# Kernel optimization log

Measured on AMD Instinct MI355X. Metric: run time of the kernel, lower is better.

## Reference

```python
import jax, jax.numpy as jnp
import numpy as np

B, N, F, D, M, R, K, TOPR = 32, 1024, 10, 64, 4, 8, 20, 2
TAU = 1.0
BN_EPS = 1e-5


def setup_inputs() -> dict:
    key = jax.random.key(0)
    ks = jax.random.split(key, 20)
    s = 0.1
    p = {}
    p['data'] = jax.random.normal(ks[0], (B, N, F), jnp.float32)
    u = jnp.clip(jax.random.uniform(ks[1], (B, M), jnp.float32), 1e-6, 1.0 - 1e-6)
    p['gumbel_noise'] = -jnp.log(-jnp.log(u))
    p['W_cond'] = jax.random.normal(ks[2], (F, D), jnp.float32) * s
    p['b_cond'] = jnp.zeros((D,), jnp.float32)
    p['W_ap'] = jax.random.normal(ks[3], (D, D), jnp.float32) * s
    p['b_ap'] = jnp.zeros((D,), jnp.float32)
    p['W_av'] = jax.random.normal(ks[4], (D, 1), jnp.float32) * s
    p['W_r'] = jax.random.normal(ks[5], (D, M), jnp.float32) * s
    p['b_r'] = jnp.zeros((M,), jnp.float32)
    p['e_base'] = jax.random.normal(ks[6], (N, D), jnp.float32) * s
    p['lr_u'] = jax.random.normal(ks[7], (M, N, R), jnp.float32) * s
    p['lr_v'] = jax.random.normal(ks[8], (M, R, D), jnp.float32) * s
    p['W_gnn'] = jax.random.normal(ks[9], (F, D), jnp.float32) * s
    p['att_i'] = jax.random.normal(ks[10], (D,), jnp.float32) * s
    p['att_j'] = jax.random.normal(ks[11], (D,), jnp.float32) * s
    p['att_em_i'] = jax.random.normal(ks[12], (D,), jnp.float32) * s
    p['att_em_j'] = jax.random.normal(ks[13], (D,), jnp.float32) * s
    p['b_gnn'] = jnp.zeros((D,), jnp.float32)
    p['bn1_gamma'] = jnp.ones((D,), jnp.float32)
    p['bn1_beta'] = jnp.zeros((D,), jnp.float32)
    p['node_embed_table'] = jax.random.normal(ks[14], (N, D), jnp.float32) * s
    p['bn_out_gamma'] = jnp.ones((D,), jnp.float32)
    p['bn_out_beta'] = jnp.zeros((D,), jnp.float32)
    p['W_out'] = jax.random.normal(ks[15], (D, 1), jnp.float32) * s
    p['b_out'] = jnp.zeros((1,), jnp.float32)
    return p


def _nan(x):
    return jnp.nan_to_num(x, nan=0.0, posinf=1e4, neginf=-1e4)


def _bn(x, gamma, beta, axes):
    # BatchNorm1d in training mode: biased batch stats over `axes`.
    mu = x.mean(axes, keepdims=True)
    var = x.var(axes, keepdims=True)
    return (x - mu) * jax.lax.rsqrt(var + BN_EPS) * gamma + beta


def reference(data, gumbel_noise, W_cond, b_cond, W_ap, b_ap, W_av, W_r, b_r,
              e_base, lr_u, lr_v, W_gnn, att_i, att_j, att_em_i, att_em_j,
              b_gnn, bn1_gamma, bn1_beta, node_embed_table,
              bn_out_gamma, bn_out_beta, W_out, b_out):
    x_det = jax.lax.stop_gradient(data)                      # data.clone().detach()
    # --- condition attention pooling ---
    h_it = data @ W_cond + b_cond                            # [B,N,D]
    ah = jax.nn.leaky_relu(h_it @ W_ap + b_ap, 0.2)
    e_it = _nan((ah @ W_av)[..., 0])                         # [B,N]
    beta = jax.nn.softmax(e_it, axis=1)
    h_sys = jnp.sum(beta[..., None] * h_it, axis=1)          # [B,D]
    # --- gumbel top-k routing with straight-through ---
    pi_soft = jax.nn.softmax((h_sys @ W_r + b_r + gumbel_noise) / TAU, axis=-1)
    topv, topi = jax.lax.top_k(pi_soft, TOPR)
    pi_hard = jnp.sum(jax.nn.one_hot(topi, M, dtype=pi_soft.dtype) * topv[..., None], axis=1)
    pi_hard = pi_hard / jnp.maximum(pi_hard.sum(-1, keepdims=True), 1e-12)
    pi_t = jax.lax.stop_gradient(pi_hard - pi_soft) + pi_soft
    # --- low-rank expert prototypes -> mixed node embeddings ---
    proto = e_base[None] + jnp.einsum('mnr,mrd->mnd', lr_u, lr_v)    # [M,N,D]
    mixed = _nan(jnp.einsum('bm,mnd->bnd', pi_t, proto))             # [B,N,D]
    # --- dynamic top-k graph construction ---
    scores = _nan(jnp.einsum('bid,bjd->bij', mixed, mixed))          # [B,N,N]
    topk_vals, topk_idx = jax.lax.top_k(scores, K)                   # src nodes per dst: [B,N,K]
    topk_w = jax.nn.softmax(topk_vals, axis=-1)                      # edge weights
    # --- GAT-style layer with embedding-augmented keys, self loops re-added ---
    x_lin = x_det @ W_gnn                                            # [B,N,D]
    s_i = x_lin @ att_i + mixed @ att_em_i                           # [B,N]
    s_j = x_lin @ att_j + mixed @ att_em_j
    sj_nb = jnp.take_along_axis(s_j, topk_idx.reshape(B, N * K), axis=1).reshape(B, N, K)
    self_mask = topk_idx == jnp.arange(N)[None, :, None]             # remove_self_loops on topk edges
    alpha_nb = jnp.where(self_mask, -jnp.inf, jax.nn.leaky_relu(s_i[:, :, None] + sj_nb, 0.2))
    alpha_self = jax.nn.leaky_relu(s_i + s_j, 0.2)
    att = jax.nn.softmax(jnp.concatenate([alpha_nb, alpha_self[..., None]], axis=-1), axis=-1)
    w_nb = att[..., :K] * topk_w                                     # edge_weight modulation
    w_self = att[..., K]
    x_src = jnp.take_along_axis(x_lin, topk_idx.reshape(B, N * K)[..., None], axis=1).reshape(B, N, K, D)
    gnn = jnp.einsum('bnk,bnkd->bnd', w_nb, x_src) + w_self[..., None] * x_lin + b_gnn
    gnn = jax.nn.relu(_bn(gnn.reshape(B * N, D), bn1_gamma, bn1_beta, 0).reshape(B, N, D))
    # --- output head ---
    out = gnn * node_embed_table[None]                               # [B,N,D]
    out = jax.nn.relu(_bn(out, bn_out_gamma, bn_out_beta, (0, 1)))   # dropout = identity (eval)
    out = (out @ W_out + b_out).reshape(-1, N)                       # [B,N]
    return out, h_sys, pi_soft
```

## Files before the change

### kernel.cpp

```cpp
#include <hip/hip_runtime.h>
#include <math.h>

#define BB 32
#define NN 1024
#define FF 10
#define DD 64
#define MM 4
#define RR 8
#define KK 20
#define BNROWS (BB*NN)

#define OFF_HIT   0ull
#define OFF_XLIN  2097152ull
#define OFF_EIT   4194304ull
#define OFF_PIT   4227072ull
#define OFF_MIXED 4227200ull
#define OFF_SI    6324352ull
#define OFF_SJ    6357120ull
#define OFF_GNN   7700608ull
#define OFF_OUTP  9797760ull
#define OFF_STAT  11894912ull
#define OFF_SC    (OFF_STAT + 2560ull)

__device__ __forceinline__ float wave_sum(float v) {
    #pragma unroll
    for (int off = 32; off; off >>= 1) v += __shfl_xor(v, off);
    return v;
}
__device__ __forceinline__ float wave_max(float v) {
    #pragma unroll
    for (int off = 32; off; off >>= 1) v = fmaxf(v, __shfl_xor(v, off));
    return v;
}

__global__ __launch_bounds__(256) void k_rows(
    const float* __restrict__ data, const float* __restrict__ W_cond,
    const float* __restrict__ b_cond, const float* __restrict__ W_ap,
    const float* __restrict__ b_ap, const float* __restrict__ W_av,
    const float* __restrict__ W_gnn,
    float* __restrict__ h_it, float* __restrict__ x_lin, float* __restrict__ e_it,
    float* __restrict__ stats)
{
    if (blockIdx.x < 10) {
        int idx = blockIdx.x * 256 + threadIdx.x;
        if (idx < 2336) stats[idx] = 0.f;
    }
    int w = threadIdx.x >> 6, lane = threadIdx.x & 63;
    int r = blockIdx.x * 4 + w;
    const float* dr = data + r * FF;
    float df[FF];
    #pragma unroll
    for (int f = 0; f < FF; f++) df[f] = dr[f];
    float h = b_cond[lane], x = 0.f;
    #pragma unroll
    for (int f = 0; f < FF; f++) {
        h = fmaf(df[f], W_cond[f * DD + lane], h);
        x = fmaf(df[f], W_gnn[f * DD + lane], x);
    }
    h_it[r * DD + lane] = h;
    x_lin[r * DD + lane] = x;
    float acc = b_ap[lane];
    #pragma unroll
    for (int e2 = 0; e2 < DD; e2++)
        acc = fmaf(__shfl(h, e2), W_ap[e2 * DD + lane], acc);
    float lr = acc > 0.f ? acc : 0.2f * acc;
    float ep = wave_sum(lr * W_av[lane]);
    if (lane == 0) e_it[r] = ep;
}

__global__ __launch_bounds__(256) void k_pool2(
    const float* __restrict__ e_it, const float* __restrict__ h_it,
    float* __restrict__ num, float* __restrict__ den)
{
    int w = threadIdx.x >> 6, lane = threadIdx.x & 63;
    int b = blockIdx.x >> 3, ch = blockIdx.x & 7;
    int base = b * NN + ch * 128 + w * 32;
    float acc = 0.f, dn = 0.f;
    #pragma unroll 4
    for (int i = 0; i < 32; i++) {
        float e = e_it[base + i];
        float wgt = expf(e);
        acc = fmaf(wgt, h_it[(size_t)(base + i) * DD + lane], acc);
        dn += wgt;
    }
    __shared__ float pa[4][DD];
    __shared__ float pd[4];
    pa[w][lane] = acc;
    if (lane == 0) pd[w] = dn;
    __syncthreads();
    if (w == 0) {
        float s = pa[0][lane] + pa[1][lane] + pa[2][lane] + pa[3][lane];
        atomicAdd(&num[b * DD + lane], s);
        if (lane == 0) atomicAdd(&den[b], pd[0] + pd[1] + pd[2] + pd[3]);
    }
}

__global__ void k_route(const float* __restrict__ num, const float* __restrict__ den,
                        const float* __restrict__ W_r, const float* __restrict__ b_r,
                        const float* __restrict__ gumbel,
                        float* __restrict__ h_sys, float* __restrict__ pi_soft,
                        float* __restrict__ pi_t)
{
    int tid = threadIdx.x;
    for (int i = tid; i < BB * DD; i += 256)
        h_sys[i] = num[i] / den[i >> 6];
    if (tid >= BB) return;
    int b = tid;
    float inv = 1.0f / den[b];
    float lg[MM];
    #pragma unroll
    for (int m = 0; m < MM; m++) lg[m] = b_r[m] + gumbel[b * MM + m];
    for (int d = 0; d < DD; d++) {
        float hv = num[b * DD + d] * inv;
        #pragma unroll
        for (int m = 0; m < MM; m++) lg[m] = fmaf(hv, W_r[d * MM + m], lg[m]);
    }
    float mx = fmaxf(fmaxf(lg[0], lg[1]), fmaxf(lg[2], lg[3]));
    float s = 0.f, p[MM];
    #pragma unroll
    for (int m = 0; m < MM; m++) { p[m] = expf(lg[m] - mx); s += p[m]; }
    #pragma unroll
    for (int m = 0; m < MM; m++) { p[m] /= s; pi_soft[b * MM + m] = p[m]; }
    int i1 = 0; float v1 = p[0];
    #pragma unroll
    for (int m = 1; m < MM; m++) if (p[m] > v1) { v1 = p[m]; i1 = m; }
    int i2 = -1; float v2 = -1.f;
    #pragma unroll
    for (int m = 0; m < MM; m++) if (m != i1 && p[m] > v2) { v2 = p[m]; i2 = m; }
    float norm = fmaxf(v1 + v2, 1e-12f);
    #pragma unroll
    for (int m = 0; m < MM; m++)
        pi_t[b * MM + m] = (m == i1 ? v1 : (m == i2 ? v2 : 0.f)) / norm;
}

__global__ __launch_bounds__(256) void k_mixed(
    const float* __restrict__ e_base, const float* __restrict__ lr_u,
    const float* __restrict__ lr_v, const float* __restrict__ pi_t,
    const float* __restrict__ x_lin,
    const float* __restrict__ att_i, const float* __restrict__ att_j,
    const float* __restrict__ att_em_i, const float* __restrict__ att_em_j,
    float* __restrict__ mixed, float* __restrict__ s_i, float* __restrict__ s_j)
{
    int w = threadIdx.x >> 6, lane = threadIdx.x & 63;
    int r = blockIdx.x * 4 + w;
    int b = r >> 10, n = r & 1023;
    float LR[MM];
    #pragma unroll
    for (int m = 0; m < MM; m++) {
        float a = 0.f;
        #pragma unroll
        for (int rr = 0; rr < RR; rr++)
            a = fmaf(lr_u[(m * NN + n) * RR + rr], lr_v[(m * RR + rr) * DD + lane], a);
        LR[m] = a;
    }
    float eb = e_base[n * DD + lane];
    float mx = 0.f;
    #pragma unroll
    for (int m = 0; m < MM; m++) mx = fmaf(pi_t[b * MM + m], eb + LR[m], mx);
    mixed[(size_t)r * DD + lane] = mx;
    float x = x_lin[(size_t)r * DD + lane];
    float r1 = wave_sum(x * att_i[lane] + mx * att_em_i[lane]);
    float r2 = wave_sum(x * att_j[lane] + mx * att_em_j[lane]);
    if (lane == 0) { s_i[r] = r1; s_j[r] = r2; }
}

__global__ __launch_bounds__(256) void k_score(
    const float* __restrict__ mixed_chunk, float* __restrict__ sc)
{
    __shared__ float As[32 * 132];
    __shared__ float Bs[32 * 132];
    int t = threadIdx.x;
    int bb = blockIdx.x >> 6;
    int rr = blockIdx.x & 63;
    int it = rr >> 3, jt = rr & 7;
    int i0 = it * 128, j0 = jt * 128;
    const float* mb = mixed_chunk + (size_t)bb * NN * DD;

    int tx = t & 15, ty = t >> 4;
    float acc[8][8];
    #pragma unroll
    for (int a = 0; a < 8; a++)
        #pragma unroll
        for (int bj = 0; bj < 8; bj++) acc[a][bj] = 0.f;

    int rowi[4], qi[4], swi[4];
    #pragma unroll
    for (int c = 0; c < 4; c++) {
        int id = t + c * 256;
        rowi[c] = (id & 15) | ((id >> 7) << 4);
        qi[c] = (id >> 4) & 7;
        swi[c] = ((rowi[c] & 4) << 4) | ((rowi[c] >> 3) << 2) | (rowi[c] & 3);
    }

    float4 pa[4], pb[4];
    #pragma unroll
    for (int c = 0; c < 4; c++) {
        pa[c] = *(const float4*)(mb + (size_t)(i0 + rowi[c]) * DD + qi[c] * 4);
        pb[c] = *(const float4*)(mb + (size_t)(j0 + rowi[c]) * DD + qi[c] * 4);
    }
    for (int hh = 0; hh < 2; hh++) {
        if (hh) __syncthreads();
        #pragma unroll
        for (int c = 0; c < 4; c++) {
            int pos = qi[c] * 4 * 132 + swi[c];
            As[pos] = pa[c].x; As[pos + 132] = pa[c].y; As[pos + 264] = pa[c].z; As[pos + 396] = pa[c].w;
            Bs[pos] = pb[c].x; Bs[pos + 132] = pb[c].y; Bs[pos + 264] = pb[c].z; Bs[pos + 396] = pb[c].w;
        }
        __syncthreads();
        if (hh == 0) {
            #pragma unroll
            for (int c = 0; c < 4; c++) {
                pa[c] = *(const float4*)(mb + (size_t)(i0 + rowi[c]) * DD + 32 + qi[c] * 4);
                pb[c] = *(const float4*)(mb + (size_t)(j0 + rowi[c]) * DD + 32 + qi[c] * 4);
            }
        }
        #pragma unroll 4
        for (int d = 0; d < 32; d++) {
            float4 a0 = *(const float4*)&As[d * 132 + ty * 4];
            float4 a1 = *(const float4*)&As[d * 132 + 64 + ty * 4];
            float4 b0 = *(const float4*)&Bs[d * 132 + tx * 4];
            float4 b1 = *(const float4*)&Bs[d * 132 + 64 + tx * 4];
            float av[8] = {a0.x, a0.y, a0.z, a0.w, a1.x, a1.y, a1.z, a1.w};
            float bv[8] = {b0.x, b0.y, b0.z, b0.w, b1.x, b1.y, b1.z, b1.w};
            #pragma unroll
            for (int a = 0; a < 8; a++)
                #pragma unroll
                for (int bj = 0; bj < 8; bj++)
                    acc[a][bj] = fmaf(av[a], bv[bj], acc[a][bj]);
        }
    }

    float* out = sc + ((size_t)bb * NN + i0 + ty * 8) * NN + j0 + tx * 8;
    #pragma unroll
    for (int a = 0; a < 8; a++) {
        float4 o0 = {acc[a][0], acc[a][1], acc[a][2], acc[a][3]};
        float4 o1 = {acc[a][4], acc[a][5], acc[a][6], acc[a][7]};
        *(float4*)(out + (size_t)a * NN) = o0;
        *(float4*)(out + (size_t)a * NN + 4) = o1;
    }
}

__global__ __launch_bounds__(256) void k_selgat(
    const float* __restrict__ sc, int b0,
    const float* __restrict__ x_lin, const float* __restrict__ s_i,
    const float* __restrict__ s_j, const float* __restrict__ b_gnn,
    float* __restrict__ gnn_pre)
{
    int w = threadIdx.x >> 6, lane = threadIdx.x & 63;
    int lr = blockIdx.x * 4 + w;
    int r = b0 * NN + lr;
    int b = r >> 10, n = r & 1023;
    const float* row = sc + (size_t)lr * NN;

    unsigned uk[16];
    #pragma unroll
    for (int c = 0; c < 4; c++) {
        float4 v = *(const float4*)(row + c * 256 + lane * 4);
        float vv[4] = {v.x, v.y, v.z, v.w};
        #pragma unroll
        for (int q = 0; q < 4; q++) {
            unsigned u = __float_as_uint(vv[q]);
            uk[c * 4 + q] = u ^ (((unsigned)((int)u >> 31)) | 0x80000000u);
        }
    }
    unsigned mx = uk[0];
    #pragma unroll
    for (int i = 1; i < 16; i++) mx = uk[i] > mx ? uk[i] : mx;
    unsigned sv = mx;
    #pragma unroll
    for (int blk = 2; blk <= 64; blk <<= 1) {
        #pragma unroll
        for (int dist = blk >> 1; dist >= 1; dist >>= 1) {
            unsigned pv = (unsigned)__shfl_xor((int)sv, dist);
            bool up = (lane & blk) == 0;
            bool upper = (lane & dist) == 0;
            bool g = sv > pv;
            sv = (((g == upper) == up)) ? sv : pv;
        }
    }
    unsigned tau = (unsigned)__shfl((int)sv, 19);

    __shared__ unsigned skey[4][64];
    __shared__ int sjj[4][64];
    int base = 0;
    #pragma unroll
    for (int s = 0; s < 16; s++) {
        bool q = uk[s] >= tau;
        unsigned long long m = __ballot(q);
        if (q) {
            int pos = base + __popcll(m & ((1ull << lane) - 1ull));
            if (pos < 64) {
                skey[w][pos] = uk[s];
                sjj[w][pos] = ((s >> 2) << 8) + lane * 4 + (s & 3);
            }
        }
        base += __popcll(m);
    }
    int C = base;

    float vk = -INFINITY; int ik = 0;
    if (C <= 64) {
        unsigned ck = 0u; int cj = 0x7FFFFFFF;
        if (lane < C) { ck = skey[w][lane]; cj = sjj[w][lane]; }
        if (C <= 32) {
            #pragma unroll
            for (int blk = 2; blk <= 32; blk <<= 1)
                #pragma unroll
                for (int dist = blk >> 1; dist >= 1; dist >>= 1) {
                    unsigned pk = (unsigned)__shfl_xor((int)ck, dist);
                    int pj = __shfl_xor(cj, dist);
                    bool up = (lane & blk) == 0;
                    bool upper = (lane & dist) == 0;
                    bool g = (ck > pk) || (ck == pk && cj < pj);
                    bool keep = ((g == upper) == up);
                    ck = keep ? ck : pk; cj = keep ? cj : pj;
                }
        } else {
            #pragma unroll
            for (int blk = 2; blk <= 64; blk <<= 1)
                #pragma unroll
                for (int dist = blk >> 1; dist >= 1; dist >>= 1) {
                    unsigned pk = (unsigned)__shfl_xor((int)ck, dist);
                    int pj = __shfl_xor(cj, dist);
                    bool up = (lane & blk) == 0;
                    bool upper = (lane & dist) == 0;
                    bool g = (ck > pk) || (ck == pk && cj < pj);
                    bool keep = ((g == upper) == up);
                    ck = keep ? ck : pk; cj = keep ? cj : pj;
                }
        }
        if (lane < KK) {
            unsigned u = (ck & 0x80000000u) ? (ck ^ 0x80000000u) : ~ck;
            vk = __uint_as_float(u);
            ik = cj;
        }
    } else {
        for (int k = 0; k < KK; k++) {
            unsigned bm = uk[0]; int bsl = 0;
            #pragma unroll
            for (int i = 1; i < 16; i++) if (uk[i] > bm) { bm = uk[i]; bsl = i; }
            unsigned wm = bm;
            #pragma unroll
            for (int off = 32; off; off >>= 1) {
                unsigned tt = (unsigned)__shfl_xor((int)wm, off);
                wm = tt > wm ? tt : wm;
            }
            unsigned long long ball = __ballot(bm == wm);
            int winner = (int)__builtin_ctzll(ball);
            int slotw = __shfl(bsl, winner);
            int jw = ((slotw >> 2) << 8) + winner * 4 + (slotw & 3);
            unsigned u2 = (wm & 0x80000000u) ? (wm ^ 0x80000000u) : ~wm;
            if (lane == k) { vk = __uint_as_float(u2); ik = jw; }
            if (lane == winner) uk[bsl] = 0u;
        }
    }

    float m1 = wave_max(vk);
    float ek = (lane < KK) ? expf(vk - m1) : 0.f;
    float s1v = wave_sum(ek);
    float wk = ek / s1v;
    float si = s_i[r], sjn = s_j[r];
    float a = -INFINITY;
    if (lane < KK) {
        float sjk = s_j[(b << 10) + ik];
        float t2 = si + sjk;
        a = (ik == n) ? -INFINITY : (t2 > 0.f ? t2 : 0.2f * t2);
    }
    float ts = si + sjn;
    float aself = ts > 0.f ? ts : 0.2f * ts;
    float am = wave_max(fmaxf(a, aself));
    float ea = (lane < KK && a != -INFINITY) ? expf(a - am) : 0.f;
    float es = expf(aself - am);
    float ssum = wave_sum(ea) + es;
    float wnb = (ea / ssum) * wk;
    float wself = es / ssum;
    float acc = b_gnn[lane] + wself * x_lin[(size_t)r * DD + lane];
    #pragma unroll
    for (int k = 0; k < KK; k++) {
        int jk = __shfl(ik, k);
        float wv = __shfl(wnb, k);
        acc = fmaf(wv, x_lin[((size_t)(b << 10) + jk) * DD + lane], acc);
    }
    gnn_pre[(size_t)r * DD + lane] = acc;
}

__global__ __launch_bounds__(256) void k_stats(const float* __restrict__ src, float* __restrict__ sums)
{
    int w = threadIdx.x >> 6, lane = threadIdx.x & 63;
    __shared__ float ps[4][DD], pq[4][DD];
    float s = 0.f, q = 0.f;
    int base = blockIdx.x * 128;
    for (int i = w; i < 128; i += 4) {
        float v = src[(size_t)(base + i) * DD + lane];
        s += v; q = fmaf(v, v, q);
    }
    ps[w][lane] = s; pq[w][lane] = q;
    __syncthreads();
    if (w == 0) {
        s = ps[0][lane] + ps[1][lane] + ps[2][lane] + ps[3][lane];
        q = pq[0][lane] + pq[1][lane] + pq[2][lane] + pq[3][lane];
        atomicAdd(&sums[lane], s);
        atomicAdd(&sums[DD + lane], q);
    }
}

__global__ __launch_bounds__(256) void k_bn1(
    const float* __restrict__ gnn_pre, float* __restrict__ stats,
    const float* __restrict__ gamma, const float* __restrict__ beta,
    const float* __restrict__ net, float* __restrict__ out_pre)
{
    int tid = threadIdx.x;
    int d0 = (tid & 15) * 4;
    float mean4[4], rs4[4], bt4[4];
    #pragma unroll
    for (int k = 0; k < 4; k++) {
        float mu = stats[d0 + k] * (1.0f / BNROWS);
        float var = stats[64 + d0 + k] * (1.0f / BNROWS) - mu * mu;
        mean4[k] = mu;
        rs4[k] = rsqrtf(var + 1e-5f) * gamma[d0 + k];
        bt4[k] = beta[d0 + k];
    }
    float s4[4] = {0, 0, 0, 0}, q4[4] = {0, 0, 0, 0};
    size_t base4 = (size_t)blockIdx.x * 2048;
    #pragma unroll
    for (int i = 0; i < 8; i++) {
        size_t f4 = base4 + (size_t)i * 256 + tid;
        float4 v = ((const float4*)gnn_pre)[f4];
        int n = ((int)(f4 >> 4)) & 1023;
        float4 nv = ((const float4*)net)[(size_t)n * 16 + (tid & 15)];
        float vv[4] = {v.x, v.y, v.z, v.w};
        float nn2[4] = {nv.x, nv.y, nv.z, nv.w};
        float ov[4];
        #pragma unroll
        for (int k = 0; k < 4; k++) {
            float y = (vv[k] - mean4[k]) * rs4[k] + bt4[k];
            y = y > 0.f ? y : 0.f;
            float o = y * nn2[k];
            ov[k] = o;
            s4[k] += o;
            q4[k] = fmaf(o, o, q4[k]);
        }
        float4 o4 = {ov[0], ov[1], ov[2], ov[3]};
        ((float4*)out_pre)[f4] = o4;
    }
    __shared__ float4 ls[256], lq[256];
    ls[tid] = make_float4(s4[0], s4[1], s4[2], s4[3]);
    lq[tid] = make_float4(q4[0], q4[1], q4[2], q4[3]);
    __syncthreads();
    if (tid < 16) {
        float4 S = ls[tid], Q = lq[tid];
        #pragma unroll
        for (int rr = 1; rr < 16; rr++) {
            float4 a = ls[tid + 16 * rr], b = lq[tid + 16 * rr];
            S.x += a.x; S.y += a.y; S.z += a.z; S.w += a.w;
            Q.x += b.x; Q.y += b.y; Q.z += b.z; Q.w += b.w;
        }
        atomicAdd(&stats[128 + tid * 4 + 0], S.x);
        atomicAdd(&stats[128 + tid * 4 + 1], S.y);
        atomicAdd(&stats[128 + tid * 4 + 2], S.z);
        atomicAdd(&stats[128 + tid * 4 + 3], S.w);
        atomicAdd(&stats[192 + tid * 4 + 0], Q.x);
        atomicAdd(&stats[192 + tid * 4 + 1], Q.y);
        atomicAdd(&stats[192 + tid * 4 + 2], Q.z);
        atomicAdd(&stats[192 + tid * 4 + 3], Q.w);
    }
}

__global__ __launch_bounds__(256) void k_head(
    const float* __restrict__ out_pre, const float* __restrict__ stats,
    const float* __restrict__ gamma, const float* __restrict__ beta,
    const float* __restrict__ W_out, const float* __restrict__ b_out,
    float* __restrict__ out)
{
    int w = threadIdx.x >> 6, lane = threadIdx.x & 63;
    int r = blockIdx.x * 4 + w;
    float mean = stats[lane] * (1.0f / BNROWS);
    float var = stats[DD + lane] * (1.0f / BNROWS) - mean * mean;
    float rs = rsqrtf(var + 1e-5f);
    float y = (out_pre[(size_t)r * DD + lane] - mean) * rs * gamma[lane] + beta[lane];
    y = y > 0.f ? y : 0.f;
    float p = wave_sum(y * W_out[lane]);
    if (lane == 0) out[r] = p + b_out[0];
}

extern "C" void kernel_launch(void* const* d_in, const int* in_sizes, int n_in,
                              void* d_out, int out_size, void* d_ws, size_t ws_size,
                              hipStream_t stream)
{
    const float* data     = (const float*)d_in[0];
    const float* gumbel   = (const float*)d_in[1];
    const float* W_cond   = (const float*)d_in[2];
    const float* b_cond   = (const float*)d_in[3];
    const float* W_ap     = (const float*)d_in[4];
    const float* b_ap     = (const float*)d_in[5];
    const float* W_av     = (const float*)d_in[6];
    const float* W_r      = (const float*)d_in[7];
    const float* b_r      = (const float*)d_in[8];
    const float* e_base   = (const float*)d_in[9];
    const float* lr_u     = (const float*)d_in[10];
    const float* lr_v     = (const float*)d_in[11];
    const float* W_gnn    = (const float*)d_in[12];
    const float* att_i    = (const float*)d_in[13];
    const float* att_j    = (const float*)d_in[14];
    const float* att_em_i = (const float*)d_in[15];
    const float* att_em_j = (const float*)d_in[16];
    const float* b_gnn    = (const float*)d_in[17];
    const float* bn1_g    = (const float*)d_in[18];
    const float* bn1_b    = (const float*)d_in[19];
    const float* net      = (const float*)d_in[20];
    const float* bno_g    = (const float*)d_in[21];
    const float* bno_b    = (const float*)d_in[22];
    const float* W_out    = (const float*)d_in[23];
    const float* b_out    = (const float*)d_in[24];

    float* ws = (float*)d_ws;
    float* h_it   = ws + OFF_HIT;
    float* x_lin  = ws + OFF_XLIN;
    float* e_it   = ws + OFF_EIT;
    float* pi_t   = ws + OFF_PIT;
    float* mixed  = ws + OFF_MIXED;
    float* s_i    = ws + OFF_SI;
    float* s_j    = ws + OFF_SJ;
    float* gnn_pre = ws + OFF_GNN;
    float* out_pre = ws + OFF_OUTP;
    float* stats   = ws + OFF_STAT;
    float* pnum    = stats + 256;
    float* pden    = stats + 2304;

    float* out0    = (float*)d_out;
    float* h_sys   = out0 + BB * NN;
    float* pi_soft = out0 + BB * NN + BB * DD;

    k_rows<<<BNROWS / 4, 256, 0, stream>>>(data, W_cond, b_cond, W_ap, b_ap, W_av, W_gnn,
                                           h_it, x_lin, e_it, stats);
    k_pool2<<<BB * 8, 256, 0, stream>>>(e_it, h_it, pnum, pden);
    k_route<<<1, 256, 0, stream>>>(pnum, pden, W_r, b_r, gumbel, h_sys, pi_soft, pi_t);
    k_mixed<<<BNROWS / 4, 256, 0, stream>>>(e_base, lr_u, lr_v, pi_t, x_lin,
                                            att_i, att_j, att_em_i, att_em_j, mixed, s_i, s_j);

    size_t ws_floats = ws_size / 4;
    size_t avail = ws_floats > OFF_SC ? ws_floats - OFF_SC : 0;
    int cb = (int)(avail / (size_t)(NN * NN));
    if (cb > BB) cb = BB;
    float* sc = ws + OFF_SC;
    if (cb < 1) { cb = 2; sc = h_it; }
    for (int b0 = 0; b0 < BB; b0 += cb) {
        int c = (BB - b0) < cb ? (BB - b0) : cb;
        k_score<<<c * 64, 256, 0, stream>>>(mixed + (size_t)b0 * NN * DD, sc);
        k_selgat<<<c * 256, 256, 0, stream>>>(sc, b0, x_lin, s_i, s_j, b_gnn, gnn_pre);
    }

    k_stats<<<256, 256, 0, stream>>>(gnn_pre, stats);
    k_bn1<<<256, 256, 0, stream>>>(gnn_pre, stats, bn1_g, bn1_b, net, out_pre);
    k_head<<<BNROWS / 4, 256, 0, stream>>>(out_pre, stats + 128, bno_g, bno_b, W_out, b_out, out0);
}
```

Baseline: 327.1 us.

## Fuse score GEMM, top-k selection, GAT aggregation and BN stats into one kernel

Replaces the separate score GEMM, top-k/GAT kernel and stats kernel with one fused kernel. Each 512-thread block computes a 32x1024 similarity strip and keeps it in registers, with a transposed shared-memory B tile, then runs top-k, attention and aggregation directly on those registers. Batch-norm sums are accumulated in the same kernel. This removes the large N×N score matrix round trip through global memory and two kernel launches. In exchange it uses a large shared-memory footprint and 64 accumulators per thread, which may limit occupancy, and the transposed shared-memory stores may hit bank conflicts.

Measured after the change: 373.6 us. 14.2% more time.

```diff
diff --git a/kernel.cpp b/kernel.cpp
--- a/kernel.cpp
+++ b/kernel.cpp
@@ -20,7 +20,6 @@
 #define OFF_GNN   7700608ull
 #define OFF_OUTP  9797760ull
 #define OFF_STAT  11894912ull
-#define OFF_SC    (OFF_STAT + 2560ull)
 
 __device__ __forceinline__ float wave_sum(float v) {
     #pragma unroll
@@ -164,243 +163,223 @@
     if (lane == 0) { s_i[r] = r1; s_j[r] = r2; }
 }
 
-__global__ __launch_bounds__(256) void k_score(
-    const float* __restrict__ mixed_chunk, float* __restrict__ sc)
-{
-    __shared__ float As[32 * 132];
-    __shared__ float Bs[32 * 132];
+__global__ __launch_bounds__(512) void k_fused(
+    const float* __restrict__ mixed, const float* __restrict__ x_lin,
+    const float* __restrict__ s_i, const float* __restrict__ s_j,
+    const float* __restrict__ b_gnn, float* __restrict__ gnn_pre,
+    float* __restrict__ stats)
+{
+    __shared__ float As[32 * DD];
+    __shared__ float BT[DD * 256];
+
     int t = threadIdx.x;
-    int bb = blockIdx.x >> 6;
-    int rr = blockIdx.x & 63;
-    int it = rr >> 3, jt = rr & 7;
-    int i0 = it * 128, j0 = jt * 128;
-    const float* mb = mixed_chunk + (size_t)bb * NN * DD;
-
-    int tx = t & 15, ty = t >> 4;
-    float acc[8][8];
-    #pragma unroll
-    for (int a = 0; a < 8; a++)
-        #pragma unroll
-        for (int bj = 0; bj < 8; bj++) acc[a][bj] = 0.f;
-
-    int rowi[4], qi[4], swi[4];
+    int w = t >> 6, lane = t & 63;
+    int b = blockIdx.x >> 5;
+    int it = blockIdx.x & 31;
+    int i0 = it * 32;
+    const float* mb = mixed + (size_t)b * NN * DD;
+
+    *(float4*)&As[t * 4] = *(const float4*)(mb + (size_t)i0 * DD + t * 4);
+
+    float acc[4][16];
+    #pragma unroll
+    for (int a = 0; a < 4; a++)
+        #pragma unroll
+        for (int s = 0; s < 16; s++) acc[a][s] = 0.f;
+
+    int jl = t >> 1;
+    int dh = (t & 1) * 32;
+    int rbase = w * 4;
+
+    const float4* BT4 = (const float4*)BT;
+    const float4* As4 = (const float4*)As;
+
     #pragma unroll
     for (int c = 0; c < 4; c++) {
-        int id = t + c * 256;
-        rowi[c] = (id & 15) | ((id >> 7) << 4);
-        qi[c] = (id >> 4) & 7;
-        swi[c] = ((rowi[c] & 4) << 4) | ((rowi[c] >> 3) << 2) | (rowi[c] & 3);
-    }
-
-    float4 pa[4], pb[4];
-    #pragma unroll
-    for (int c = 0; c < 4; c++) {
-        pa[c] = *(const float4*)(mb + (size_t)(i0 + rowi[c]) * DD + qi[c] * 4);
-        pb[c] = *(const float4*)(mb + (size_t)(j0 + rowi[c]) * DD + qi[c] * 4);
-    }
-    for (int hh = 0; hh < 2; hh++) {
-        if (hh) __syncthreads();
-        #pragma unroll
-        for (int c = 0; c < 4; c++) {
-            int pos = qi[c] * 4 * 132 + swi[c];
-            As[pos] = pa[c].x; As[pos + 132] = pa[c].y; As[pos + 264] = pa[c].z; As[pos + 396] = pa[c].w;
-            Bs[pos] = pb[c].x; Bs[pos + 132] = pb[c].y; Bs[pos + 264] = pb[c].z; Bs[pos + 396] = pb[c].w;
-        }
         __syncthreads();
-        if (hh == 0) {
+        const float* src = mb + (size_t)(c * 256 + jl) * DD + dh;
+        #pragma unroll
+        for (int i = 0; i < 8; i++) {
+            float4 v = *(const float4*)(src + i * 4);
+            int d0 = dh + i * 4;
+            BT[(d0 + 0) * 256 + jl] = v.x;
+            BT[(d0 + 1) * 256 + jl] = v.y;
+            BT[(d0 + 2) * 256 + jl] = v.z;
+            BT[(d0 + 3) * 256 + jl] = v.w;
+        }
+        __syncthreads();
+        #pragma unroll 4
+        for (int d4 = 0; d4 < 16; d4++) {
+            float4 b0 = BT4[(d4 * 4 + 0) * 64 + lane];
+            float4 b1 = BT4[(d4 * 4 + 1) * 64 + lane];
+            float4 b2 = BT4[(d4 * 4 + 2) * 64 + lane];
+            float4 b3 = BT4[(d4 * 4 + 3) * 64 + lane];
             #pragma unroll
-            for (int c = 0; c < 4; c++) {
-                pa[c] = *(const float4*)(mb + (size_t)(i0 + rowi[c]) * DD + 32 + qi[c] * 4);
-                pb[c] = *(const float4*)(mb + (size_t)(j0 + rowi[c]) * DD + 32 + qi[c] * 4);
-            }
-        }
-        #pragma unroll 4
-        for (int d = 0; d < 32; d++) {
-            float4 a0 = *(const float4*)&As[d * 132 + ty * 4];
-            float4 a1 = *(const float4*)&As[d * 132 + 64 + ty * 4];
-            float4 b0 = *(const float4*)&Bs[d * 132 + tx * 4];
-            float4 b1 = *(const float4*)&Bs[d * 132 + 64 + tx * 4];
-            float av[8] = {a0.x, a0.y, a0.z, a0.w, a1.x, a1.y, a1.z, a1.w};
-            float bv[8] = {b0.x, b0.y, b0.z, b0.w, b1.x, b1.y, b1.z, b1.w};
+            for (int rr = 0; rr < 4; rr++) {
+                float4 a = As4[(rbase + rr) * 16 + d4];
+                acc[rr][c * 4 + 0] = fmaf(a.w, b3.x, fmaf(a.z, b2.x, fmaf(a.y, b1.x, fmaf(a.x, b0.x, acc[rr][c * 4 + 0]))));
+                acc[rr][c * 4 + 1] = fmaf(a.w, b3.y, fmaf(a.z, b2.y, fmaf(a.y, b1.y, fmaf(a.x, b0.y, acc[rr][c * 4 + 1]))));
+                acc[rr][c * 4 + 2] = fmaf(a.w, b3.z, fmaf(a.z, b2.z, fmaf(a.y, b1.z, fmaf(a.x, b0.z, acc[rr][c * 4 + 2]))));
+                acc[rr][c * 4 + 3] = fmaf(a.w, b3.w, fmaf(a.z, b2.w, fmaf(a.y, b1.w, fmaf(a.x, b0.w, acc[rr][c * 4 + 3]))));
+            }
+        }
+    }
+    __syncthreads();
+
+    unsigned* skeyW = (unsigned*)&BT[w * 64];
+    int*      sjjW  = (int*)&BT[512 + w * 64];
+
+    float ssum = 0.f, qsum = 0.f;
+
+    #pragma unroll 1
+    for (int rr = 0; rr < 4; rr++) {
+        int n = i0 + rbase + rr;
+        int r = (b << 10) + n;
+
+        unsigned uk[16];
+        #define EXTRACT_ROW(RRC) \
+            _Pragma("unroll") \
+            for (int s = 0; s < 16; s++) { \
+                unsigned u = __float_as_uint(acc[RRC][s]); \
+                uk[s] = u ^ (((unsigned)((int)u >> 31)) | 0x80000000u); \
+            }
+        if (rr == 0)      { EXTRACT_ROW(0) }
+        else if (rr == 1) { EXTRACT_ROW(1) }
+        else if (rr == 2) { EXTRACT_ROW(2) }
+        else              { EXTRACT_ROW(3) }
+
+        unsigned mx = uk[0];
+        #pragma unroll
+        for (int i = 1; i < 16; i++) mx = uk[i] > mx ? uk[i] : mx;
+        unsigned sv = mx;
+        #pragma unroll
+        for (int blk = 2; blk <= 64; blk <<= 1) {
             #pragma unroll
-            for (int a = 0; a < 8; a++)
+            for (int dist = blk >> 1; dist >= 1; dist >>= 1) {
+                unsigned pv = (unsigned)__shfl_xor((int)sv, dist);
+                bool up = (lane & blk) == 0;
+                bool upper = (lane & dist) == 0;
+                bool gt = sv > pv;
+                sv = ((gt == upper) == up) ? sv : pv;
+            }
+        }
+        unsigned tau = (unsigned)__shfl((int)sv, 19);
+
+        int base = 0;
+        #pragma unroll
+        for (int s = 0; s < 16; s++) {
+            bool q = uk[s] >= tau;
+            unsigned long long m = __ballot(q);
+            if (q) {
+                int pos = base + __popcll(m & ((1ull << lane) - 1ull));
+                if (pos < 64) {
+                    skeyW[pos] = uk[s];
+                    sjjW[pos] = ((s >> 2) << 8) + lane * 4 + (s & 3);
+                }
+            }
+            base += __popcll(m);
+        }
+        int C = base;
+
+        float vk = -INFINITY; int ik = 0;
+        if (C <= 64) {
+            unsigned ck = 0u; int cj = 0x7FFFFFFF;
+            if (lane < C) { ck = skeyW[lane]; cj = sjjW[lane]; }
+            if (C <= 32) {
                 #pragma unroll
-                for (int bj = 0; bj < 8; bj++)
-                    acc[a][bj] = fmaf(av[a], bv[bj], acc[a][bj]);
-        }
-    }
-
-    float* out = sc + ((size_t)bb * NN + i0 + ty * 8) * NN + j0 + tx * 8;
-    #pragma unroll
-    for (int a = 0; a < 8; a++) {
-        float4 o0 = {acc[a][0], acc[a][1], acc[a][2], acc[a][3]};
-        float4 o1 = {acc[a][4], acc[a][5], acc[a][6], acc[a][7]};
-        *(float4*)(out + (size_t)a * NN) = o0;
-        *(float4*)(out + (size_t)a * NN + 4) = o1;
-    }
-}
-
-__global__ __launch_bounds__(256) void k_selgat(
-    const float* __restrict__ sc, int b0,
-    const float* __restrict__ x_lin, const float* __restrict__ s_i,
-    const float* __restrict__ s_j, const float* __restrict__ b_gnn,
-    float* __restrict__ gnn_pre)
-{
-    int w = threadIdx.x >> 6, lane = threadIdx.x & 63;
-    int lr = blockIdx.x * 4 + w;
-    int r = b0 * NN + lr;
-    int b = r >> 10, n = r & 1023;
-    const float* row = sc + (size_t)lr * NN;
-
-    unsigned uk[16];
-    #pragma unroll
-    for (int c = 0; c < 4; c++) {
-        float4 v = *(const float4*)(row + c * 256 + lane * 4);
-        float vv[4] = {v.x, v.y, v.z, v.w};
-        #pragma unroll
-        for (int q = 0; q < 4; q++) {
-            unsigned u = __float_as_uint(vv[q]);
-            uk[c * 4 + q] = u ^ (((unsigned)((int)u >> 31)) | 0x80000000u);
-        }
-    }
-    unsigned mx = uk[0];
-    #pragma unroll
-    for (int i = 1; i < 16; i++) mx = uk[i] > mx ? uk[i] : mx;
-    unsigned sv = mx;
-    #pragma unroll
-    for (int blk = 2; blk <= 64; blk <<= 1) {
-        #pragma unroll
-        for (int dist = blk >> 1; dist >= 1; dist >>= 1) {
-            unsigned pv = (unsigned)__shfl_xor((int)sv, dist);
-            bool up = (lane & blk) == 0;
-            bool upper = (lane & dist) == 0;
-            bool g = sv > pv;
-            sv = (((g == upper) == up)) ? sv : pv;
-        }
-    }
-    unsigned tau = (unsigned)__shfl((int)sv, 19);
-
-    __shared__ unsigned skey[4][64];
-    __shared__ int sjj[4][64];
-    int base = 0;
-    #pragma unroll
-    for (int s = 0; s < 16; s++) {
-        bool q = uk[s] >= tau;
-        unsigned long long m = __ballot(q);
-        if (q) {
-            int pos = base + __popcll(m & ((1ull << lane) - 1ull));
-            if (pos < 64) {
-                skey[w][pos] = uk[s];
-                sjj[w][pos] = ((s >> 2) << 8) + lane * 4 + (s & 3);
-            }
-        }
-        base += __popcll(m);
-    }
-    int C = base;
-
-    float vk = -INFINITY; int ik = 0;
-    if (C <= 64) {
-        unsigned ck = 0u; int cj = 0x7FFFFFFF;
-        if (lane < C) { ck = skey[w][lane]; cj = sjj[w][lane]; }
-        if (C <= 32) {
-            #pragma unroll
-            for (int blk = 2; blk <= 32; blk <<= 1)
+                for (int blk = 2; blk <= 32; blk <<= 1)
+                    #pragma unroll
+                    for (int dist = blk >> 1; dist >= 1; dist >>= 1) {
+                        unsigned pk = (unsigned)__shfl_xor((int)ck, dist);
+                        int pj = __shfl_xor(cj, dist);
+                        bool up = (lane & blk) == 0;
+                        bool upper = (lane & dist) == 0;
+                        bool gt = (ck > pk) || (ck == pk && cj < pj);
+                        bool keep = ((gt == upper) == up);
+                        ck = keep ? ck : pk; cj = keep ? cj : pj;
+                    }
+            } else {
                 #pragma unroll
-                for (int dist = blk >> 1; dist >= 1; dist >>= 1) {
-                    unsigned pk = (unsigned)__shfl_xor((int)ck, dist);
-                    int pj = __shfl_xor(cj, dist);
-                    bool up = (lane & blk) == 0;
-                    bool upper = (lane & dist) == 0;
-                    bool g = (ck > pk) || (ck == pk && cj < pj);
-                    bool keep = ((g == upper) == up);
-                    ck = keep ? ck : pk; cj = keep ? cj : pj;
+                for (int blk = 2; blk <= 64; blk <<= 1)
+                    #pragma unroll
+                    for (int dist = blk >> 1; dist >= 1; dist >>= 1) {
+                        unsigned pk = (unsigned)__shfl_xor((int)ck, dist);
+                        int pj = __shfl_xor(cj, dist);
+                        bool up = (lane & blk) == 0;
+                        bool upper = (lane & dist) == 0;
+                        bool gt = (ck > pk) || (ck == pk && cj < pj);
+                        bool keep = ((gt == upper) == up);
+                        ck = keep ? ck : pk; cj = keep ? cj : pj;
+                    }
+            }
+            if (lane < KK) {
+                unsigned u = (ck & 0x80000000u) ? (ck ^ 0x80000000u) : ~ck;
+                vk = __uint_as_float(u);
+                ik = cj;
+            }
+        } else {
+            for (int k = 0; k < KK; k++) {
+                unsigned bm = uk[0]; int bsl = 0;
+                #pragma unroll
+                for (int i = 1; i < 16; i++) if (uk[i] > bm) { bm = uk[i]; bsl = i; }
+                unsigned wm = bm;
+                #pragma unroll
+                for (int off = 32; off; off >>= 1) {
+                    unsigned tt = (unsigned)__shfl_xor((int)wm, off);
+                    wm = tt > wm ? tt : wm;
                 }
-        } else {
-            #pragma unroll
-            for (int blk = 2; blk <= 64; blk <<= 1)
-                #pragma unroll
-                for (int dist = blk >> 1; dist >= 1; dist >>= 1) {
-                    unsigned pk = (unsigned)__shfl_xor((int)ck, dist);
-                    int pj = __shfl_xor(cj, dist);
-                    bool up = (lane & blk) == 0;
-                    bool upper = (lane & dist) == 0;
-                    bool g = (ck > pk) || (ck == pk && cj < pj);
-                    bool keep = ((g == upper) == up);
-                    ck = keep ? ck : pk; cj = keep ? cj : pj;
-                }
-        }
+                unsigned long long ball = __ballot(bm == wm);
+                int winner = (int)__builtin_ctzll(ball);
+                int slotw = __shfl(bsl, winner);
+                int jw = ((slotw >> 2) << 8) + winner * 4 + (slotw & 3);
+                unsigned u2 = (wm & 0x80000000u) ? (wm ^ 0x80000000u) : ~wm;
+                if (lane == k) { vk = __uint_as_float(u2); ik = jw; }
+                if (lane == winner) uk[bsl] = 0u;
+            }
+        }
+
+        float m1 = wave_max(vk);
+        float ek = (lane < KK) ? expf(vk - m1) : 0.f;
+        float s1v = wave_sum(ek);
+        float wk = ek / s1v;
+        float si = s_i[r], sjn = s_j[r];
+        float a = -INFINITY;
         if (lane < KK) {
-            unsigned u = (ck & 0x80000000u) ? (ck ^ 0x80000000u) : ~ck;
-            vk = __uint_as_float(u);
-            ik = cj;
-        }
-    } else {
+            float sjk = s_j[(b << 10) + ik];
+            float t2 = si + sjk;
+            a = (ik == n) ? -INFINITY : (t2 > 0.f ? t2 : 0.2f * t2);
+        }
+        float ts = si + sjn;
+        float aself = ts > 0.f ? ts : 0.2f * ts;
+        float am = wave_max(fmaxf(a, aself));
+        float ea = (lane < KK && a != -INFINITY) ? expf(a - am) : 0.f;
+        float es = expf(aself - am);
+        float sm = wave_sum(ea) + es;
+        float wnb = (ea / sm) * wk;
+        float wself = es / sm;
+        float gacc = b_gnn[lane] + wself * x_lin[(size_t)r * DD + lane];
+        #pragma unroll
         for (int k = 0; k < KK; k++) {
-            unsigned bm = uk[0]; int bsl = 0;
-            #pragma unroll
-            for (int i = 1; i < 16; i++) if (uk[i] > bm) { bm = uk[i]; bsl = i; }
-            unsigned wm = bm;
-            #pragma unroll
-            for (int off = 32; off; off >>= 1) {
-                unsigned tt = (unsigned)__shfl_xor((int)wm, off);
-                wm = tt > wm ? tt : wm;
-            }
-            unsigned long long ball = __ballot(bm == wm);
-            int winner = (int)__builtin_ctzll(ball);
-            int slotw = __shfl(bsl, winner);
-            int jw = ((slotw >> 2) << 8) + winner * 4 + (slotw & 3);
-            unsigned u2 = (wm & 0x80000000u) ? (wm ^ 0x80000000u) : ~wm;
-            if (lane == k) { vk = __uint_as_float(u2); ik = jw; }
-            if (lane == winner) uk[bsl] = 0u;
-        }
-    }
-
-    float m1 = wave_max(vk);
-    float ek = (lane < KK) ? expf(vk - m1) : 0.f;
-    float s1v = wave_sum(ek);
-    float wk = ek / s1v;
-    float si = s_i[r], sjn = s_j[r];
-    float a = -INFINITY;
-    if (lane < KK) {
-        float sjk = s_j[(b << 10) + ik];
-        float t2 = si + sjk;
-        a = (ik == n) ? -INFINITY : (t2 > 0.f ? t2 : 0.2f * t2);
-    }
-    float ts = si + sjn;
-    float aself = ts > 0.f ? ts : 0.2f * ts;
-    float am = wave_max(fmaxf(a, aself));
-    float ea = (lane < KK && a != -INFINITY) ? expf(a - am) : 0.f;
-    float es = expf(aself - am);
-    float ssum = wave_sum(ea) + es;
-    float wnb = (ea / ssum) * wk;
-    float wself = es / ssum;
-    float acc = b_gnn[lane] + wself * x_lin[(size_t)r * DD + lane];
-    #pragma unroll
-    for (int k = 0; k < KK; k++) {
-        int jk = __shfl(ik, k);
-        float wv = __shfl(wnb, k);
-        acc = fmaf(wv, x_lin[((size_t)(b << 10) + jk) * DD + lane], acc);
-    }
-    gnn_pre[(size_t)r * DD + lane] = acc;
-}
-
-__global__ __launch_bounds__(256) void k_stats(const float* __restrict__ src, float* __restrict__ sums)
-{
-    int w = threadIdx.x >> 6, lane = threadIdx.x & 63;
-    __shared__ float ps[4][DD], pq[4][DD];
-    float s = 0.f, q = 0.f;
-    int base = blockIdx.x * 128;
-    for (int i = w; i < 128; i += 4) {
-        float v = src[(size_t)(base + i) * DD + lane];
-        s += v; q = fmaf(v, v, q);
-    }
-    ps[w][lane] = s; pq[w][lane] = q;
+            int jk = __shfl(ik, k);
+            float wv = __shfl(wnb, k);
+            gacc = fmaf(wv, x_lin[((size_t)(b << 10) + jk) * DD + lane], gacc);
+        }
+        gnn_pre[(size_t)r * DD + lane] = gacc;
+        ssum += gacc;
+        qsum = fmaf(gacc, gacc, qsum);
+    }
+
+    float* ps = &BT[1024];
+    float* pq = &BT[1536];
+    ps[w * 64 + lane] = ssum;
+    pq[w * 64 + lane] = qsum;
     __syncthreads();
     if (w == 0) {
-        s = ps[0][lane] + ps[1][lane] + ps[2][lane] + ps[3][lane];
-        q = pq[0][lane] + pq[1][lane] + pq[2][lane] + pq[3][lane];
-        atomicAdd(&sums[lane], s);
-        atomicAdd(&sums[DD + lane], q);
+        float s = 0.f, q2 = 0.f;
+        #pragma unroll
+        for (int k2 = 0; k2 < 8; k2++) { s += ps[k2 * 64 + lane]; q2 += pq[k2 * 64 + lane]; }
+        atomicAdd(&stats[lane], s);
+        atomicAdd(&stats[DD + lane], q2);
     }
 }
 
@@ -537,20 +516,7 @@
     k_route<<<1, 256, 0, stream>>>(pnum, pden, W_r, b_r, gumbel, h_sys, pi_soft, pi_t);
     k_mixed<<<BNROWS / 4, 256, 0, stream>>>(e_base, lr_u, lr_v, pi_t, x_lin,
                                             att_i, att_j, att_em_i, att_em_j, mixed, s_i, s_j);
-
-    size_t ws_floats = ws_size / 4;
-    size_t avail = ws_floats > OFF_SC ? ws_floats - OFF_SC : 0;
-    int cb = (int)(avail / (size_t)(NN * NN));
-    if (cb > BB) cb = BB;
-    float* sc = ws + OFF_SC;
-    if (cb < 1) { cb = 2; sc = h_it; }
-    for (int b0 = 0; b0 < BB; b0 += cb) {
-        int c = (BB - b0) < cb ? (BB - b0) : cb;
-        k_score<<<c * 64, 256, 0, stream>>>(mixed + (size_t)b0 * NN * DD, sc);
-        k_selgat<<<c * 256, 256, 0, stream>>>(sc, b0, x_lin, s_i, s_j, b_gnn, gnn_pre);
-    }
-
-    k_stats<<<256, 256, 0, stream>>>(gnn_pre, stats);
+    k_fused<<<BB * 32, 512, 0, stream>>>(mixed, x_lin, s_i, s_j, b_gnn, gnn_pre, stats);
     k_bn1<<<256, 256, 0, stream>>>(gnn_pre, stats, bn1_g, bn1_b, net, out_pre);
     k_head<<<BNROWS / 4, 256, 0, stream>>>(out_pre, stats + 128, bno_g, bno_b, W_out, b_out, out0);
 }
```
